# Kernel tuning notes

Measured on AMD Instinct MI355X. Metric: run time of the kernel, lower is better.

The kernel has to match this reference:

```python
import jax, jax.numpy as jnp
import numpy as np

GRAD_FACTOR = 1.5
TAU = 30.0
K = 16

@jax.custom_vjp
def grad_scale(x):
    return x

def _gs_fwd(x):
    return x, None

def _gs_bwd(_, g):
    return (g * GRAD_FACTOR,)

grad_scale.defvjp(_gs_fwd, _gs_bwd)


def logic_layer(x, idx, w):
    # x: [..., D]; idx: [2, out] int; w: [out, 16]
    # difflogic soft logic layer: softmax over the 16 two-input boolean ops.
    x = grad_scale(x)
    a = x[..., idx[0]]
    b = x[..., idx[1]]
    ab = a * b
    ops = jnp.stack([
        jnp.zeros_like(a),          # 0: FALSE
        ab,                         # 1: a AND b
        a - ab,                     # 2: a AND NOT b
        a,                          # 3: a
        b - ab,                     # 4: NOT a AND b
        b,                          # 5: b
        a + b - 2 * ab,             # 6: XOR
        a + b - ab,                 # 7: OR
        1 - (a + b - ab),           # 8: NOR
        1 - (a + b - 2 * ab),       # 9: XNOR
        1 - b,                      # 10: NOT b
        1 - b + ab,                 # 11: a OR NOT b
        1 - a,                      # 12: NOT a
        1 - a + ab,                 # 13: NOT a OR b
        1 - ab,                     # 14: NAND
        jnp.ones_like(a),           # 15: TRUE
    ], axis=-1)                     # [..., out, 16]
    p = jax.nn.softmax(w, axis=-1)  # [out, 16]
    return jnp.einsum('...ok,ok->...o', ops, p)


def logic_tree(xp, i0, w0, i1, w1, i2, w2):
    # depth-3 tree: in_dim -> 4 -> 2 -> 1
    h = logic_layer(xp, i0, w0)
    h = logic_layer(h, i1, w1)
    h = logic_layer(h, i2, w2)
    return h[..., 0]


def conv(x, params, ksize, stride, pad):
    # per-filter logic-tree conv (unfold + vmapped trees over out_channels)
    B, C, H, W = x.shape
    xp = jnp.pad(x, ((0, 0), (0, 0), (pad, pad), (pad, pad)))
    oh = (H + 2 * pad - ksize) // stride + 1
    ow = (W + 2 * pad - ksize) // stride + 1
    # patches ordered channel-major then (ki, kj), matching F.unfold
    pat = jnp.stack([xp[:, :, i:i + oh * stride:stride, j:j + ow * stride:stride]
                     for i in range(ksize) for j in range(ksize)], axis=2)  # [B,C,k*k,oh,ow]
    pat = pat.reshape(B, C * ksize * ksize, oh * ow).transpose(0, 2, 1)
    pat = pat.reshape(B * oh * ow, C * ksize * ksize)  # [(B*L), C*k*k]
    # vmap over filters: idx [2,F,d], w [F,d,16]
    out = jax.vmap(logic_tree, in_axes=(None, 1, 0, 1, 0, 1, 0))(pat, *params)  # [F, B*L]
    return out.reshape(-1, B, oh, ow).transpose(1, 0, 2, 3)


def orpool(x):
    return jax.lax.reduce_window(x, -jnp.inf, jax.lax.max, (1, 1, 2, 2), (1, 1, 2, 2), 'VALID')


def _tree_params(rng, in_dim, n_filters):
    dims = [(in_dim, 4), (4, 2), (2, 1)]
    out = []
    for d_in, d_out in dims:
        idx = rng.randint(0, d_in, size=(2, n_filters, d_out)).astype(np.int32)
        w = (0.1 * rng.randn(n_filters, d_out, 16)).astype(np.float32)
        w[..., 3] += 5.0  # 'residual' init favors pass-through op
        out += [jnp.asarray(idx), jnp.asarray(w)]
    return out


def _fc_params(rng, d_in, d_out):
    idx = rng.randint(0, d_in, size=(2, d_out)).astype(np.int32)
    w = (0.1 * rng.randn(d_out, 16)).astype(np.float32)
    w[..., 3] += 5.0
    return jnp.asarray(idx), jnp.asarray(w)


def setup_inputs() -> dict:
    key = jax.random.key(0)
    rng = np.random.RandomState(0)
    inp = {"x": jax.random.uniform(key, (100, 1, 28, 28), dtype=jnp.float32)}
    for name, in_dim, f in [("c1", 25, K), ("c2", 9 * K, 3 * K), ("c3", 27 * K, 9 * K)]:
        p = _tree_params(rng, in_dim, f)
        for li in range(3):
            inp[f"{name}_idx{li}"] = p[2 * li]
            inp[f"{name}_w{li}"] = p[2 * li + 1]
    for name, d_in, d_out in [("fc1", 81 * K, 1280 * K), ("fc2", 1280 * K, 640 * K), ("fc3", 640 * K, 320 * K)]:
        idx, w = _fc_params(rng, d_in, d_out)
        inp[f"{name}_idx"] = idx
        inp[f"{name}_w"] = w
    return inp


def reference(x,
              c1_idx0, c1_w0, c1_idx1, c1_w1, c1_idx2, c1_w2,
              c2_idx0, c2_w0, c2_idx1, c2_w1, c2_idx2, c2_w2,
              c3_idx0, c3_w0, c3_idx1, c3_w1, c3_idx2, c3_w2,
              fc1_idx, fc1_w, fc2_idx, fc2_w, fc3_idx, fc3_w):
    x = (x > 0.5).astype(jnp.float32)
    x = conv(x, (c1_idx0, c1_w0, c1_idx1, c1_w1, c1_idx2, c1_w2), 5, 1, 0)
    x = orpool(x)
    x = conv(x, (c2_idx0, c2_w0, c2_idx1, c2_w1, c2_idx2, c2_w2), 3, 1, 1)
    x = orpool(x)
    x = conv(x, (c3_idx0, c3_w0, c3_idx1, c3_w1, c3_idx2, c3_w2), 3, 1, 1)
    x = orpool(x)
    B = x.shape[0]
    x = x.reshape(B, -1)  # [B, 81*K]
    x = logic_layer(x, fc1_idx, fc1_w)
    x = logic_layer(x, fc2_idx, fc2_w)
    x = logic_layer(x, fc3_idx, fc3_w)
    # GroupSum(k=10, tau=30)
    return x.reshape(B, 10, -1).sum(-1) / TAU
```

## Files before the change

kernel.cpp:

```cpp
#include <hip/hip_runtime.h>
#include <hip/hip_fp16.h>
#include <math.h>

#define DEV __device__ __forceinline__

DEV float gev(float4 c, float a, float b) {
    return fmaf(c.w, a * b, fmaf(c.z, b, fmaf(c.y, a, c.x)));
}

struct __align__(16) FcRec {
    __half2 c01, c23;
    unsigned int idx;
    unsigned int pad;
};

DEV float4 softmax_coef(const float* __restrict__ wrow) {
    const float4* wv = (const float4*)wrow;
    float4 q0 = wv[0], q1 = wv[1], q2 = wv[2], q3 = wv[3];
    float p[16] = {q0.x,q0.y,q0.z,q0.w, q1.x,q1.y,q1.z,q1.w,
                   q2.x,q2.y,q2.z,q2.w, q3.x,q3.y,q3.z,q3.w};
    float mx = p[0];
    #pragma unroll
    for (int k = 1; k < 16; k++) mx = fmaxf(mx, p[k]);
    float s = 0.f;
    #pragma unroll
    for (int k = 0; k < 16; k++) { p[k] = __expf(p[k] - mx); s += p[k]; }
    float inv = 1.f / s;
    #pragma unroll
    for (int k = 0; k < 16; k++) p[k] *= inv;
    float c0  = p[8]+p[9]+p[10]+p[11]+p[12]+p[13]+p[14]+p[15];
    float ca  = p[2]+p[3]+p[6]+p[7]-p[8]-p[9]-p[12]-p[13];
    float cb  = p[4]+p[5]+p[6]+p[7]-p[8]-p[9]-p[10]-p[11];
    float cab = p[1]-p[2]-p[4]-2.f*p[6]-p[7]+p[8]+2.f*p[9]+p[11]+p[13]-p[14];
    return make_float4(c0, ca, cb, cab);
}

DEV float4 onehot4(int i) {
    return make_float4(i == 0 ? 1.f : 0.f, i == 1 ? 1.f : 0.f,
                       i == 2 ? 1.f : 0.f, i == 3 ? 1.f : 0.f);
}

__global__ __launch_bounds__(256) void setup_kernel(
    const int* __restrict__ c1i0, const int* __restrict__ c1i1, const int* __restrict__ c1i2,
    const int* __restrict__ c2i0, const int* __restrict__ c2i1, const int* __restrict__ c2i2,
    const int* __restrict__ c3i0, const int* __restrict__ c3i1, const int* __restrict__ c3i2,
    const float* __restrict__ c1w0, const float* __restrict__ c1w1, const float* __restrict__ c1w2,
    const float* __restrict__ c2w0, const float* __restrict__ c2w1, const float* __restrict__ c2w2,
    const float* __restrict__ c3w0, const float* __restrict__ c3w1, const float* __restrict__ c3w2,
    const int* __restrict__ fc1i, const float* __restrict__ fc1w,
    const int* __restrict__ fc2i, const float* __restrict__ fc2w,
    const int* __restrict__ fc3i, const float* __restrict__ fc3w,
    FcRec* __restrict__ fcp1, FcRec* __restrict__ fcp2, FcRec* __restrict__ fcp3,
    float4* __restrict__ cvp)
{
    int t = blockIdx.x * 256 + threadIdx.x;
    if (t >= 36048) return;
    if (t < 35840) {
        const float* w; const int* idx; FcRec* dst; int o, D;
        if (t < 20480)      { o = t;         D = 20480; w = fc1w; idx = fc1i; dst = fcp1; }
        else if (t < 30720) { o = t - 20480; D = 10240; w = fc2w; idx = fc2i; dst = fcp2; }
        else                { o = t - 30720; D = 5120;  w = fc3w; idx = fc3i; dst = fcp3; }
        float4 cf = softmax_coef(w + o * 16);
        FcRec r;
        r.c01 = __half2(__float2half_rn(cf.x), __float2half_rn(cf.y));
        r.c23 = __half2(__float2half_rn(cf.z), __float2half_rn(cf.w));
        r.idx = ((unsigned)idx[o] & 0xffffu) | ((unsigned)idx[D + o] << 16);
        r.pad = 0;
        dst[o] = r;
        return;
    }
    int f = t - 35840;
    const int *i0, *i1, *i2; const float *W0, *W1, *W2;
    int F, KS, mode, lf;
    if (f < 16)      { lf = f;      F = 16;  KS = 5; mode = 1;
                       i0 = c1i0; i1 = c1i1; i2 = c1i2; W0 = c1w0; W1 = c1w1; W2 = c1w2; }
    else if (f < 64) { lf = f - 16; F = 48;  KS = 3; mode = 2;
                       i0 = c2i0; i1 = c2i1; i2 = c2i2; W0 = c2w0; W1 = c2w1; W2 = c2w2; }
    else             { lf = f - 64; F = 144; KS = 3; mode = 3;
                       i0 = c3i0; i1 = c3i1; i2 = c3i2; W0 = c3w0; W1 = c3w1; W2 = c3w2; }
    float4* pk = cvp + f * 14;
    int offs[8];
    #pragma unroll
    for (int g = 0; g < 8; g++) {
        int tt = (g < 4) ? i0[lf * 4 + g] : i0[F * 4 + lf * 4 + (g - 4)];
        int kk = KS * KS;
        int c = tt / kk, r = tt - c * kk;
        int dy = r / KS, dx = r - dy * KS;
        int off;
        if (mode == 1)      off = dy * 28 + dx;
        else if (mode == 2) off = (c * 14 + dy) * 14 + dx;
        else                off = (c * 8 + dy) * 8 + dx;
        offs[g] = off;
    }
    ((int4*)pk)[0] = make_int4(offs[0], offs[1], offs[2], offs[3]);
    ((int4*)pk)[1] = make_int4(offs[4], offs[5], offs[6], offs[7]);
    #pragma unroll
    for (int g = 0; g < 4; g++) pk[2 + g] = softmax_coef(W0 + (lf * 4 + g) * 16);
    pk[6] = onehot4(i1[lf * 2 + 0]);
    pk[7] = onehot4(i1[F * 2 + lf * 2 + 0]);
    pk[8] = onehot4(i1[lf * 2 + 1]);
    pk[9] = onehot4(i1[F * 2 + lf * 2 + 1]);
    pk[10] = softmax_coef(W1 + (lf * 2 + 0) * 16);
    pk[11] = softmax_coef(W1 + (lf * 2 + 1) * 16);
    int a2 = i2[lf], b2 = i2[F + lf];
    pk[12] = make_float4(a2 == 0 ? 1.f : 0.f, a2 == 1 ? 1.f : 0.f,
                         b2 == 0 ? 1.f : 0.f, b2 == 1 ? 1.f : 0.f);
    pk[13] = softmax_coef(W2 + lf * 16);
}

template <int PITCH, int HP, int F, int OUTP>
DEV void conv_stage(const float* Sin, float* Sout, const float4* __restrict__ pack,
                    int tid)
{
    constexpr int N = F * HP * HP;
    for (int t = tid; t < N; t += 1024) {
        int f  = t / (HP * HP);
        int p  = t - f * (HP * HP);
        int ph = p / HP, pw = p - ph * HP;
        const float4* pk = pack + f * 14;
        int4 ao = ((const int4*)pk)[0];
        int4 bo = ((const int4*)pk)[1];
        int base0 = 2 * ph * PITCH + 2 * pw;
        int offs[8] = {ao.x, ao.y, ao.z, ao.w, bo.x, bo.y, bo.z, bo.w};
        float v[8][4];
        #pragma unroll
        for (int g = 0; g < 8; g++) {
            const float* q = Sin + offs[g] + base0;
            v[g][0] = q[0];
            v[g][1] = q[1];
            v[g][2] = q[PITCH];
            v[g][3] = q[PITCH + 1];
        }
        float4 C00 = pk[2], C01 = pk[3], C02 = pk[4], C03 = pk[5];
        float4 oA0 = pk[6], oB0 = pk[7], oA1 = pk[8], oB1 = pk[9];
        float4 C10 = pk[10], C11 = pk[11], S2 = pk[12], C2 = pk[13];
        float m = -1e30f;
        #pragma unroll
        for (int q = 0; q < 4; q++) {
            float h00 = gev(C00, v[0][q], v[4][q]);
            float h01 = gev(C01, v[1][q], v[5][q]);
            float h02 = gev(C02, v[2][q], v[6][q]);
            float h03 = gev(C03, v[3][q], v[7][q]);
            float sa0 = fmaf(oA0.x, h00, fmaf(oA0.y, h01, fmaf(oA0.z, h02, oA0.w * h03)));
            float sb0 = fmaf(oB0.x, h00, fmaf(oB0.y, h01, fmaf(oB0.z, h02, oB0.w * h03)));
            float sa1 = fmaf(oA1.x, h00, fmaf(oA1.y, h01, fmaf(oA1.z, h02, oA1.w * h03)));
            float sb1 = fmaf(oB1.x, h00, fmaf(oB1.y, h01, fmaf(oB1.z, h02, oB1.w * h03)));
            float h10 = gev(C10, sa0, sb0);
            float h11 = gev(C11, sa1, sb1);
            float vv = gev(C2, fmaf(S2.x, h10, S2.y * h11),
                               fmaf(S2.z, h10, S2.w * h11));
            m = fmaxf(m, vv);
        }
        if (OUTP)
            Sout[(f * OUTP + ph + 1) * OUTP + (pw + 1)] = m;
        else
            Sout[t] = m;
    }
}

__global__ __launch_bounds__(1024, 4) void conv_kernel(
    const float* __restrict__ x, const float4* __restrict__ cvp,
    float* __restrict__ P3g)
{
    __shared__ __align__(16) char S[27968];
    float* XB  = (float*)S;
    float* P1p = (float*)(S + 3136);
    float* P2p = (float*)(S + 15680);

    const int b = blockIdx.x, tid = threadIdx.x;
    if (tid < 784) XB[tid] = x[b * 784 + tid] > 0.5f ? 1.f : 0.f;
    if (tid < 784) ((float4*)P1p)[tid] = make_float4(0.f, 0.f, 0.f, 0.f);
    if (tid < 768) ((float4*)P2p)[tid] = make_float4(0.f, 0.f, 0.f, 0.f);
    __syncthreads();

    conv_stage<28, 12, 16, 14>(XB, P1p, cvp + 0 * 14, tid);
    __syncthreads();
    conv_stage<14, 6, 48, 8>(P1p, P2p, cvp + 16 * 14, tid);
    __syncthreads();
    conv_stage<8, 3, 144, 0>(P2p, P3g + b * 1296, cvp + 64 * 14, tid);
}

__global__ __launch_bounds__(1024, 4) void fc1_kernel(
    const float* __restrict__ P3g, const FcRec* __restrict__ pk,
    __half* __restrict__ F1g)
{
    __shared__ __align__(16) float Sin[1296];
    const int b = blockIdx.x / 5, s = blockIdx.x % 5, tid = threadIdx.x;
    if (tid < 648) ((float2*)Sin)[tid] = ((const float2*)(P3g + b * 1296))[tid];
    __syncthreads();
    const FcRec* p = pk + s * 4096;
    __half* dst = F1g + b * 20480 + s * 4096;
    FcRec r[4];
    #pragma unroll
    for (int j = 0; j < 4; j++) r[j] = p[tid + j * 1024];
    float va[4], vb[4];
    #pragma unroll
    for (int j = 0; j < 4; j++) {
        unsigned ii = r[j].idx;
        va[j] = Sin[ii & 0xffffu];
        vb[j] = Sin[ii >> 16];
    }
    #pragma unroll
    for (int j = 0; j < 4; j++) {
        float2 c01 = __half22float2(r[j].c01);
        float2 c23 = __half22float2(r[j].c23);
        dst[tid + j * 1024] = __float2half(
            gev(make_float4(c01.x, c01.y, c23.x, c23.y), va[j], vb[j]));
    }
}

__global__ __launch_bounds__(1024, 4) void fc2_kernel(
    const __half* __restrict__ F1g, const FcRec* __restrict__ pk,
    __half* __restrict__ F2g)
{
    __shared__ __align__(16) __half Sin[20480];
    const int b = blockIdx.x / 5, s = blockIdx.x % 5, tid = threadIdx.x;
    const int4* src = (const int4*)(F1g + b * 20480);
    #pragma unroll
    for (int i = 0; i < 3; i++) {
        int idx = tid + i * 1024;
        if (idx < 2560) ((int4*)Sin)[idx] = src[idx];
    }
    __syncthreads();
    const FcRec* p = pk + s * 2048;
    __half* dst = F2g + b * 10240 + s * 2048;
    FcRec r0 = p[tid], r1 = p[tid + 1024];
    float va0 = __half2float(Sin[r0.idx & 0xffffu]);
    float vb0 = __half2float(Sin[r0.idx >> 16]);
    float va1 = __half2float(Sin[r1.idx & 0xffffu]);
    float vb1 = __half2float(Sin[r1.idx >> 16]);
    {
        float2 c01 = __half22float2(r0.c01), c23 = __half22float2(r0.c23);
        dst[tid] = __float2half(gev(make_float4(c01.x, c01.y, c23.x, c23.y), va0, vb0));
    }
    {
        float2 c01 = __half22float2(r1.c01), c23 = __half22float2(r1.c23);
        dst[tid + 1024] = __float2half(gev(make_float4(c01.x, c01.y, c23.x, c23.y), va1, vb1));
    }
}

__global__ __launch_bounds__(1024, 4) void fc3_kernel(
    const __half* __restrict__ F2g, const FcRec* __restrict__ pk,
    float* __restrict__ out)
{
    __shared__ __align__(16) __half Sin[10240];
    __shared__ float red[16];
    const int b = blockIdx.x / 5, s = blockIdx.x % 5, tid = threadIdx.x;
    const int4* src = (const int4*)(F2g + b * 10240);
    #pragma unroll
    for (int i = 0; i < 2; i++) {
        int idx = tid + i * 1024;
        if (idx < 1280) ((int4*)Sin)[idx] = src[idx];
    }
    __syncthreads();
    FcRec r = pk[s * 1024 + tid];
    float va = __half2float(Sin[r.idx & 0xffffu]);
    float vb = __half2float(Sin[r.idx >> 16]);
    float2 c01 = __half22float2(r.c01), c23 = __half22float2(r.c23);
    float v = gev(make_float4(c01.x, c01.y, c23.x, c23.y), va, vb);
    #pragma unroll
    for (int off = 32; off > 0; off >>= 1) v += __shfl_down(v, off, 64);
    int wave = tid >> 6, lane = tid & 63;
    if (lane == 0) red[wave] = v;
    __syncthreads();
    if (tid < 2) {
        float ssum = 0.f;
        #pragma unroll
        for (int i = 0; i < 8; i++) ssum += red[tid * 8 + i];
        out[b * 10 + 2 * s + tid] = ssum * (1.f / 30.f);
    }
}

extern "C" void kernel_launch(void* const* d_in, const int* in_sizes, int n_in,
                              void* d_out, int out_size, void* d_ws, size_t ws_size,
                              hipStream_t stream)
{
    const float* x     = (const float*)d_in[0];
    const int*   c1i0  = (const int*)d_in[1];  const float* c1w0 = (const float*)d_in[2];
    const int*   c1i1  = (const int*)d_in[3];  const float* c1w1 = (const float*)d_in[4];
    const int*   c1i2  = (const int*)d_in[5];  const float* c1w2 = (const float*)d_in[6];
    const int*   c2i0  = (const int*)d_in[7];  const float* c2w0 = (const float*)d_in[8];
    const int*   c2i1  = (const int*)d_in[9];  const float* c2w1 = (const float*)d_in[10];
    const int*   c2i2  = (const int*)d_in[11]; const float* c2w2 = (const float*)d_in[12];
    const int*   c3i0  = (const int*)d_in[13]; const float* c3w0 = (const float*)d_in[14];
    const int*   c3i1  = (const int*)d_in[15]; const float* c3w1 = (const float*)d_in[16];
    const int*   c3i2  = (const int*)d_in[17]; const float* c3w2 = (const float*)d_in[18];
    const int*   fc1i  = (const int*)d_in[19]; const float* fc1w = (const float*)d_in[20];
    const int*   fc2i  = (const int*)d_in[21]; const float* fc2w = (const float*)d_in[22];
    const int*   fc3i  = (const int*)d_in[23]; const float* fc3w = (const float*)d_in[24];

    char* ws = (char*)d_ws;
    FcRec*  fcp1 = (FcRec*)ws;
    FcRec*  fcp2 = (FcRec*)(ws + 327680);
    FcRec*  fcp3 = (FcRec*)(ws + 491520);
    float4* cvp  = (float4*)(ws + 573440);
    float*  P3g  = (float*)(ws + 620032);
    __half* F1g  = (__half*)(ws + 1138432);
    __half* F2g  = (__half*)(ws + 5234432);

    setup_kernel<<<141, 256, 0, stream>>>(
        c1i0, c1i1, c1i2, c2i0, c2i1, c2i2, c3i0, c3i1, c3i2,
        c1w0, c1w1, c1w2, c2w0, c2w1, c2w2, c3w0, c3w1, c3w2,
        fc1i, fc1w, fc2i, fc2w, fc3i, fc3w,
        fcp1, fcp2, fcp3, cvp);

    conv_kernel<<<100, 1024, 0, stream>>>(x, cvp, P3g);
    fc1_kernel<<<500, 1024, 0, stream>>>(P3g, fcp1, F1g);
    fc2_kernel<<<500, 1024, 0, stream>>>(F1g, fcp2, F2g);
    fc3_kernel<<<500, 1024, 0, stream>>>(F2g, fcp3, (float*)d_out);
}
```

Measured before the change: 137.4 us.

## Fuse conv and FC kernels into one persistent kernel with paired-block sync

Replaces the separate conv, fc1, fc2 and fc3 launches with a single mega kernel. Each sample is handled by two blocks, each computing half of every stage and trading halves through global memory, with an atomic flag barrier between stages. FC activations stay in shared memory across layers. This removes three launch boundaries and gives the conv stage twice the blocks, at the cost of spin-wait barriers that rely on both blocks of a pair being resident at once, plus extra global round-trips.

```diff
diff --git a/kernel.cpp b/kernel.cpp
--- a/kernel.cpp
+++ b/kernel.cpp
@@ -38,6 +38,18 @@
 DEV float4 onehot4(int i) {
     return make_float4(i == 0 ? 1.f : 0.f, i == 1 ? 1.f : 0.f,
                        i == 2 ? 1.f : 0.f, i == 3 ? 1.f : 0.f);
+}
+
+DEV void pairsync(int* flag, int target) {
+    __syncthreads();
+    if (threadIdx.x == 0) {
+        __threadfence();
+        __hip_atomic_fetch_add(flag, 1, __ATOMIC_ACQ_REL, __HIP_MEMORY_SCOPE_AGENT);
+        while (__hip_atomic_load(flag, __ATOMIC_ACQUIRE, __HIP_MEMORY_SCOPE_AGENT) < target)
+            __builtin_amdgcn_s_sleep(1);
+    }
+    __syncthreads();
+    __threadfence();
 }
 
 __global__ __launch_bounds__(256) void setup_kernel(
@@ -51,9 +63,10 @@
     const int* __restrict__ fc2i, const float* __restrict__ fc2w,
     const int* __restrict__ fc3i, const float* __restrict__ fc3w,
     FcRec* __restrict__ fcp1, FcRec* __restrict__ fcp2, FcRec* __restrict__ fcp3,
-    float4* __restrict__ cvp)
+    float4* __restrict__ cvp, int* __restrict__ flags)
 {
     int t = blockIdx.x * 256 + threadIdx.x;
+    if (t < 1600) flags[t] = 0;
     if (t >= 36048) return;
     if (t < 35840) {
         const float* w; const int* idx; FcRec* dst; int o, D;
@@ -108,14 +121,15 @@
     pk[13] = softmax_coef(W2 + lf * 16);
 }
 
-template <int PITCH, int HP, int F, int OUTP>
-DEV void conv_stage(const float* Sin, float* Sout, const float4* __restrict__ pack,
-                    int tid)
-{
-    constexpr int N = F * HP * HP;
+template <int PITCH, int HP, int OUTP, int NF>
+DEV void conv_half(const float* Sin, float* SoutL, float* __restrict__ SoutG,
+                   const float4* __restrict__ pack, int f0, int tid)
+{
+    constexpr int N = NF * HP * HP;
     for (int t = tid; t < N; t += 1024) {
-        int f  = t / (HP * HP);
-        int p  = t - f * (HP * HP);
+        int fl = t / (HP * HP);
+        int p  = t - fl * (HP * HP);
+        int f  = f0 + fl;
         int ph = p / HP, pw = p - ph * HP;
         const float4* pk = pack + f * 14;
         int4 ao = ((const int4*)pk)[0];
@@ -152,122 +166,146 @@
             m = fmaxf(m, vv);
         }
         if (OUTP)
-            Sout[(f * OUTP + ph + 1) * OUTP + (pw + 1)] = m;
+            SoutL[(f * OUTP + ph + 1) * OUTP + (pw + 1)] = m;
         else
-            Sout[t] = m;
-    }
-}
-
-__global__ __launch_bounds__(1024, 4) void conv_kernel(
+            SoutL[f * HP * HP + p] = m;
+        SoutG[f * HP * HP + p] = m;
+    }
+}
+
+template <int HP, int OUTP, int NF>
+DEV void stage_pad(const float* __restrict__ G, float* L, int f0, int tid)
+{
+    constexpr int N = NF * HP * HP;
+    for (int t = tid; t < N; t += 1024) {
+        int fl = t / (HP * HP);
+        int p  = t - fl * (HP * HP);
+        int f  = f0 + fl;
+        int ph = p / HP, pw = p - ph * HP;
+        L[(f * OUTP + ph + 1) * OUTP + (pw + 1)] = G[f * HP * HP + p];
+    }
+}
+
+template <int DOUT, int CH, typename TIN>
+DEV void fc_dual(const TIN* Sin, __half* __restrict__ Dg, __half* Dl,
+                 const FcRec* __restrict__ pk, int tid)
+{
+    constexpr int K = DOUT / 1024;
+    #pragma unroll 1
+    for (int k0 = 0; k0 < K; k0 += CH) {
+        FcRec r[CH];
+        #pragma unroll
+        for (int j = 0; j < CH; j++) r[j] = pk[tid + (k0 + j) * 1024];
+        float va[CH], vb[CH];
+        #pragma unroll
+        for (int j = 0; j < CH; j++) {
+            unsigned ii = r[j].idx;
+            va[j] = (float)Sin[ii & 0xffffu];
+            vb[j] = (float)Sin[ii >> 16];
+        }
+        #pragma unroll
+        for (int j = 0; j < CH; j++) {
+            float2 c01 = __half22float2(r[j].c01);
+            float2 c23 = __half22float2(r[j].c23);
+            float4 c = make_float4(c01.x, c01.y, c23.x, c23.y);
+            __half v = __float2half(gev(c, va[j], vb[j]));
+            Dg[tid + (k0 + j) * 1024] = v;
+            Dl[tid + (k0 + j) * 1024] = v;
+        }
+    }
+}
+
+__global__ __launch_bounds__(1024, 4) void mega_kernel(
     const float* __restrict__ x, const float4* __restrict__ cvp,
-    float* __restrict__ P3g)
-{
-    __shared__ __align__(16) char S[27968];
-    float* XB  = (float*)S;
-    float* P1p = (float*)(S + 3136);
-    float* P2p = (float*)(S + 15680);
-
-    const int b = blockIdx.x, tid = threadIdx.x;
-    if (tid < 784) XB[tid] = x[b * 784 + tid] > 0.5f ? 1.f : 0.f;
+    const FcRec* __restrict__ fcp1, const FcRec* __restrict__ fcp2,
+    const FcRec* __restrict__ fcp3,
+    float* __restrict__ P1g, float* __restrict__ P2g, float* __restrict__ P3g,
+    __half* __restrict__ F1g, __half* __restrict__ F2g,
+    int* __restrict__ flags, float* __restrict__ out)
+{
+    __shared__ __align__(16) char S[66624];
+    __shared__ float red[48];
+    __half* F1s = (__half*)S;
+    float*  P2p = (float*)S;
+    float*  P1p = (float*)(S + 12544);
+    float*  XB  = (float*)(S + 25600);
+    __half* F2s = (__half*)(S + 40960);
+    float*  P3s = (float*)(S + 61440);
+
+    const int tid = threadIdx.x;
+    const int i = blockIdx.x >> 1, h = blockIdx.x & 1;
+    int* flag = flags + i * 16;
+
+    if (tid < 784) XB[tid] = x[i * 784 + tid] > 0.5f ? 1.f : 0.f;
     if (tid < 784) ((float4*)P1p)[tid] = make_float4(0.f, 0.f, 0.f, 0.f);
     if (tid < 768) ((float4*)P2p)[tid] = make_float4(0.f, 0.f, 0.f, 0.f);
     __syncthreads();
 
-    conv_stage<28, 12, 16, 14>(XB, P1p, cvp + 0 * 14, tid);
-    __syncthreads();
-    conv_stage<14, 6, 48, 8>(P1p, P2p, cvp + 16 * 14, tid);
-    __syncthreads();
-    conv_stage<8, 3, 144, 0>(P2p, P3g + b * 1296, cvp + 64 * 14, tid);
-}
-
-__global__ __launch_bounds__(1024, 4) void fc1_kernel(
-    const float* __restrict__ P3g, const FcRec* __restrict__ pk,
-    __half* __restrict__ F1g)
-{
-    __shared__ __align__(16) float Sin[1296];
-    const int b = blockIdx.x / 5, s = blockIdx.x % 5, tid = threadIdx.x;
-    if (tid < 648) ((float2*)Sin)[tid] = ((const float2*)(P3g + b * 1296))[tid];
-    __syncthreads();
-    const FcRec* p = pk + s * 4096;
-    __half* dst = F1g + b * 20480 + s * 4096;
-    FcRec r[4];
-    #pragma unroll
-    for (int j = 0; j < 4; j++) r[j] = p[tid + j * 1024];
-    float va[4], vb[4];
-    #pragma unroll
-    for (int j = 0; j < 4; j++) {
-        unsigned ii = r[j].idx;
-        va[j] = Sin[ii & 0xffffu];
-        vb[j] = Sin[ii >> 16];
-    }
-    #pragma unroll
-    for (int j = 0; j < 4; j++) {
-        float2 c01 = __half22float2(r[j].c01);
-        float2 c23 = __half22float2(r[j].c23);
-        dst[tid + j * 1024] = __float2half(
-            gev(make_float4(c01.x, c01.y, c23.x, c23.y), va[j], vb[j]));
-    }
-}
-
-__global__ __launch_bounds__(1024, 4) void fc2_kernel(
-    const __half* __restrict__ F1g, const FcRec* __restrict__ pk,
-    __half* __restrict__ F2g)
-{
-    __shared__ __align__(16) __half Sin[20480];
-    const int b = blockIdx.x / 5, s = blockIdx.x % 5, tid = threadIdx.x;
-    const int4* src = (const int4*)(F1g + b * 20480);
-    #pragma unroll
-    for (int i = 0; i < 3; i++) {
-        int idx = tid + i * 1024;
-        if (idx < 2560) ((int4*)Sin)[idx] = src[idx];
-    }
-    __syncthreads();
-    const FcRec* p = pk + s * 2048;
-    __half* dst = F2g + b * 10240 + s * 2048;
-    FcRec r0 = p[tid], r1 = p[tid + 1024];
-    float va0 = __half2float(Sin[r0.idx & 0xffffu]);
-    float vb0 = __half2float(Sin[r0.idx >> 16]);
-    float va1 = __half2float(Sin[r1.idx & 0xffffu]);
-    float vb1 = __half2float(Sin[r1.idx >> 16]);
+    conv_half<28, 12, 14, 8>(XB, P1p, P1g + i * 2304, cvp, h * 8, tid);
+    pairsync(flag, 2);
+    stage_pad<12, 14, 8>(P1g + i * 2304, P1p, (1 - h) * 8, tid);
+    __syncthreads();
+
+    conv_half<14, 6, 8, 24>(P1p, P2p, P2g + i * 1728, cvp + 16 * 14, h * 24, tid);
+    pairsync(flag, 4);
+    stage_pad<6, 8, 24>(P2g + i * 1728, P2p, (1 - h) * 24, tid);
+    __syncthreads();
+
+    conv_half<8, 3, 0, 72>(P2p, P3s, P3g + i * 1296, cvp + 64 * 14, h * 72, tid);
+    pairsync(flag, 6);
     {
-        float2 c01 = __half22float2(r0.c01), c23 = __half22float2(r0.c23);
-        dst[tid] = __float2half(gev(make_float4(c01.x, c01.y, c23.x, c23.y), va0, vb0));
-    }
+        int o = (1 - h) * 648;
+        for (int k = tid; k < 648; k += 1024) P3s[o + k] = P3g[i * 1296 + o + k];
+    }
+    __syncthreads();
+
+    fc_dual<10240, 10, float>(P3s, F1g + i * 20480 + h * 10240,
+                              F1s + h * 10240, fcp1 + h * 10240, tid);
+    pairsync(flag, 8);
     {
-        float2 c01 = __half22float2(r1.c01), c23 = __half22float2(r1.c23);
-        dst[tid + 1024] = __float2half(gev(make_float4(c01.x, c01.y, c23.x, c23.y), va1, vb1));
-    }
-}
-
-__global__ __launch_bounds__(1024, 4) void fc3_kernel(
-    const __half* __restrict__ F2g, const FcRec* __restrict__ pk,
-    float* __restrict__ out)
-{
-    __shared__ __align__(16) __half Sin[10240];
-    __shared__ float red[16];
-    const int b = blockIdx.x / 5, s = blockIdx.x % 5, tid = threadIdx.x;
-    const int4* src = (const int4*)(F2g + b * 10240);
-    #pragma unroll
-    for (int i = 0; i < 2; i++) {
-        int idx = tid + i * 1024;
-        if (idx < 1280) ((int4*)Sin)[idx] = src[idx];
-    }
-    __syncthreads();
-    FcRec r = pk[s * 1024 + tid];
-    float va = __half2float(Sin[r.idx & 0xffffu]);
-    float vb = __half2float(Sin[r.idx >> 16]);
-    float2 c01 = __half22float2(r.c01), c23 = __half22float2(r.c23);
-    float v = gev(make_float4(c01.x, c01.y, c23.x, c23.y), va, vb);
-    #pragma unroll
-    for (int off = 32; off > 0; off >>= 1) v += __shfl_down(v, off, 64);
-    int wave = tid >> 6, lane = tid & 63;
-    if (lane == 0) red[wave] = v;
-    __syncthreads();
-    if (tid < 2) {
-        float ssum = 0.f;
-        #pragma unroll
-        for (int i = 0; i < 8; i++) ssum += red[tid * 8 + i];
-        out[b * 10 + 2 * s + tid] = ssum * (1.f / 30.f);
+        int o4 = (1 - h) * 1280;
+        const int4* src = (const int4*)(F1g + i * 20480);
+        int4* dst = (int4*)F1s;
+        for (int k = tid; k < 1280; k += 1024) dst[o4 + k] = src[o4 + k];
+    }
+    __syncthreads();
+
+    fc_dual<5120, 5, __half>(F1s, F2g + i * 10240 + h * 5120,
+                             F2s + h * 5120, fcp2 + h * 5120, tid);
+    pairsync(flag, 10);
+    {
+        int o4 = (1 - h) * 640;
+        const int4* src = (const int4*)(F2g + i * 10240);
+        int4* dst = (int4*)F2s;
+        for (int k = tid; k < 640; k += 1024) dst[o4 + k] = src[o4 + k];
+    }
+    __syncthreads();
+
+    {
+        const FcRec* pk = fcp3 + h * 2560;
+        int wave = tid >> 6, lane = tid & 63;
+        #pragma unroll
+        for (int j = 0; j < 3; j++) {
+            int l = j * 1024 + tid;
+            if (l < 2560) {
+                FcRec r = pk[l];
+                float va = __half2float(F2s[r.idx & 0xffffu]);
+                float vb = __half2float(F2s[r.idx >> 16]);
+                float2 c01 = __half22float2(r.c01), c23 = __half22float2(r.c23);
+                float v = gev(make_float4(c01.x, c01.y, c23.x, c23.y), va, vb);
+                #pragma unroll
+                for (int off = 32; off > 0; off >>= 1) v += __shfl_down(v, off, 64);
+                if (lane == 0) red[j * 16 + wave] = v;
+            }
+        }
+        __syncthreads();
+        if (tid < 5) {
+            int jj = tid >> 1, wb = (tid & 1) * 8;
+            float s = 0.f;
+            #pragma unroll
+            for (int k2 = 0; k2 < 8; k2++) s += red[jj * 16 + wb + k2];
+            out[i * 10 + h * 5 + tid] = s * (1.f / 30.f);
+        }
     }
 }
 
@@ -290,22 +328,24 @@
     const int*   fc3i  = (const int*)d_in[23]; const float* fc3w = (const float*)d_in[24];
 
     char* ws = (char*)d_ws;
-    FcRec*  fcp1 = (FcRec*)ws;
-    FcRec*  fcp2 = (FcRec*)(ws + 327680);
-    FcRec*  fcp3 = (FcRec*)(ws + 491520);
-    float4* cvp  = (float4*)(ws + 573440);
-    float*  P3g  = (float*)(ws + 620032);
-    __half* F1g  = (__half*)(ws + 1138432);
-    __half* F2g  = (__half*)(ws + 5234432);
+    FcRec*  fcp1  = (FcRec*)ws;
+    FcRec*  fcp2  = (FcRec*)(ws + 327680);
+    FcRec*  fcp3  = (FcRec*)(ws + 491520);
+    float4* cvp   = (float4*)(ws + 573440);
+    int*    flags = (int*)(ws + 620032);
+    float*  P1g   = (float*)(ws + 626432);
+    float*  P2g   = (float*)(ws + 1548032);
+    float*  P3g   = (float*)(ws + 2239232);
+    __half* F1g   = (__half*)(ws + 2757632);
+    __half* F2g   = (__half*)(ws + 6853632);
 
     setup_kernel<<<141, 256, 0, stream>>>(
         c1i0, c1i1, c1i2, c2i0, c2i1, c2i2, c3i0, c3i1, c3i2,
         c1w0, c1w1, c1w2, c2w0, c2w1, c2w2, c3w0, c3w1, c3w2,
         fc1i, fc1w, fc2i, fc2w, fc3i, fc3w,
-        fcp1, fcp2, fcp3, cvp);
-
-    conv_kernel<<<100, 1024, 0, stream>>>(x, cvp, P3g);
-    fc1_kernel<<<500, 1024, 0, stream>>>(P3g, fcp1, F1g);
-    fc2_kernel<<<500, 1024, 0, stream>>>(F1g, fcp2, F2g);
-    fc3_kernel<<<500, 1024, 0, stream>>>(F2g, fcp3, (float*)d_out);
-}
+        fcp1, fcp2, fcp3, cvp, flags);
+
+    mega_kernel<<<200, 1024, 0, stream>>>(
+        x, cvp, fcp1, fcp2, fcp3, P1g, P2g, P3g, F1g, F2g,
+        flags, (float*)d_out);
+}
```

Result: slower. 392.7 us (+185.7%).
